# Optimization experiments

Measured on AMD Instinct MI355X. Metric: run time of the kernel, lower is better.

## Reference

```python
import jax, jax.numpy as jnp
import numpy as np

N, F_IN, HID, PERIODS, E = 50000, 8, 64, 12, 1200000


def _lin_init(k, fi, fo):
    # torch.nn.Linear default init: U(-1/sqrt(fi), 1/sqrt(fi))
    s = 1.0 / np.sqrt(fi)
    k1, k2 = jax.random.split(k)
    W = jax.random.uniform(k1, (fi, fo), minval=-s, maxval=s, dtype=jnp.float32)
    b = jax.random.uniform(k2, (fo,), minval=-s, maxval=s, dtype=jnp.float32)
    return W, b


def setup_inputs() -> dict:
    key = jax.random.key(0)
    ks = jax.random.split(key, 12)
    x = jax.random.normal(ks[0], (N, F_IN, PERIODS), dtype=jnp.float32)
    edge_index = jax.random.randint(ks[1], (2, E), 0, N, dtype=jnp.int64)
    edge_attr = jax.random.uniform(ks[2], (E,), dtype=jnp.float32)
    # GCNConv weights (glorot) + zero bias
    def gcn_init(k):
        s = np.sqrt(6.0 / (F_IN + HID))
        W = jax.random.uniform(k, (F_IN, HID), minval=-s, maxval=s, dtype=jnp.float32)
        return W, jnp.zeros((HID,), jnp.float32)
    Wcz, bcz = gcn_init(ks[3])
    Wcr, bcr = gcn_init(ks[4])
    Wch, bch = gcn_init(ks[5])
    # gate linears act on cat([conv_out, H]) -> 2*HID inputs
    Wlz, blz = _lin_init(ks[6], 2 * HID, HID)
    Wlr, blr = _lin_init(ks[7], 2 * HID, HID)
    Wlh, blh = _lin_init(ks[8], 2 * HID, HID)
    # temporal attention logits (uniform init as in A3TGCN)
    attention = jax.random.uniform(ks[9], (PERIODS,), dtype=jnp.float32)
    # outer readout Linear(HID, PERIODS)
    Wout, bout = _lin_init(ks[10], HID, PERIODS)
    return {"x": x, "edge_index": edge_index, "edge_attr": edge_attr,
            "attention": attention,
            "Wcz": Wcz, "bcz": bcz, "Wcr": Wcr, "bcr": bcr, "Wch": Wch, "bch": bch,
            "Wlz": Wlz, "blz": blz, "Wlr": Wlr, "blr": blr, "Wlh": Wlh, "blh": blh,
            "Wout": Wout, "bout": bout}


def reference(x, edge_index, edge_attr, attention,
              Wcz, bcz, Wcr, bcr, Wch, bch,
              Wlz, blz, Wlr, blr, Wlh, blh,
              Wout, bout):
    n = x.shape[0]
    src, dst = edge_index[0], edge_index[1]
    # GCN symmetric normalization with self-loops (self-loop weight = 1)
    deg = jax.ops.segment_sum(edge_attr, dst, num_segments=n) + 1.0
    dinv = jax.lax.rsqrt(deg)                      # [N]
    norm = dinv[src] * edge_attr * dinv[dst]       # [E]
    self_norm = (dinv * dinv)[:, None]             # [N,1]

    def gcn(xt, W, b):
        xw = xt @ W                                # [N,HID]
        agg = jax.ops.segment_sum(xw[src] * norm[:, None], dst, num_segments=n)
        return agg + xw * self_norm + b

    H0 = jnp.zeros((n, Wcz.shape[1]), x.dtype)     # A3TGCN passes H=None each period
    probs = jax.nn.softmax(attention)

    def period_step(acc, inp):
        xt, p = inp                                # xt: [N,F_IN]
        Z = jax.nn.sigmoid(jnp.concatenate([gcn(xt, Wcz, bcz), H0], axis=1) @ Wlz + blz)
        R = jax.nn.sigmoid(jnp.concatenate([gcn(xt, Wcr, bcr), H0], axis=1) @ Wlr + blr)
        Ht = jnp.tanh(jnp.concatenate([gcn(xt, Wch, bch), H0 * R], axis=1) @ Wlh + blh)
        H = Z * H0 + (1.0 - Z) * Ht
        return acc + p * H, None

    xs = jnp.moveaxis(x, 2, 0)                     # [PERIODS, N, F_IN]
    H_accum, _ = jax.lax.scan(period_step, jnp.zeros_like(H0), (xs, probs))
    h = jax.nn.relu(H_accum)
    return h @ Wout + bout                         # [N, PERIODS]
```

## Files before the change

### kernel.cpp

```cpp
#include <hip/hip_runtime.h>
#include <hip/hip_fp16.h>
#include <cmath>

#define F_IN 8
#define PER 12
#define FEAT 96
#define HID 64
#define CAP 64
#define NB 8
#define BINBITS 8
#define NPB 256
#define BINCAP 7168
#define EPB 2048

static inline size_t al256(size_t x) { return (x + 255) & ~(size_t)255; }

__device__ __forceinline__ float frcp(float x) { return __builtin_amdgcn_rcpf(x); }

#define MIX_LO(acc, w, bits) \
    asm("v_fma_mix_f32 %0, %1, %2, %0 op_sel_hi:[0,1,0]" : "+v"(acc) : "v"(w), "v"(bits))
#define MIX_HI(acc, w, bits) \
    asm("v_fma_mix_f32 %0, %1, %2, %0 op_sel:[0,1,0] op_sel_hi:[0,1,0]" : "+v"(acc) : "v"(w), "v"(bits))


__global__ void k_weights(const float* __restrict__ Wcz, const float* __restrict__ bcz,
                          const float* __restrict__ Wch, const float* __restrict__ bch,
                          const float* __restrict__ Wlz, const float* __restrict__ blz,
                          const float* __restrict__ Wlh, const float* __restrict__ blh,
                          const float* __restrict__ att, float* __restrict__ M,
                          int* __restrict__ cursor) {
    int t = threadIdx.x;
    int j = t & 63;
    int w = t >> 6;
    cursor[t] = 0;
#pragma unroll
    for (int q = 0; q < 2; ++q) {
        int f = 2 * w + q;
        float az = 0.f, ah = 0.f;
        for (int k = 0; k < HID; ++k) {
            az = fmaf(Wcz[f * HID + k], Wlz[k * HID + j], az);
            ah = fmaf(Wch[f * HID + k], Wlh[k * HID + j], ah);
        }
        M[f * HID + j] = az;
        M[512 + f * HID + j] = ah;
    }
    if (w == 0) {
        float cz = blz[j], ch = blh[j];
        for (int k = 0; k < HID; ++k) {
            cz = fmaf(bcz[k], Wlz[k * HID + j], cz);
            ch = fmaf(bch[k], Wlh[k * HID + j], ch);
        }
        M[1024 + j] = cz;
        M[1088 + j] = ch;
        if (j < PER) {
            float s = 0.f;
            for (int tt = 0; tt < PER; ++tt) s += expf(att[tt]);
            M[1152 + j] = expf(att[j]) / s;
        }
    }
}


__global__ __launch_bounds__(256) void k_pass1(const int* __restrict__ src, const int* __restrict__ dst,
                                               const float* __restrict__ attr,
                                               int* __restrict__ cursor, int2* __restrict__ binned, int e) {
    __shared__ int hist[256];
    __shared__ int base[256];
    int t = threadIdx.x;
    int blockstart = blockIdx.x * EPB;
    hist[t] = 0;
    __syncthreads();
    int2 ent[8];
    int  br[8];
#pragma unroll
    for (int r = 0; r < 8; ++r) {
        int i = blockstart + r * 256 + t;
        if (i < e) {
            int d = dst[i];
            int b = d >> BINBITS;
            int rank = atomicAdd(&hist[b], 1);
            ent[r].x = src[i] | ((d & 255) << 20);
            ent[r].y = __float_as_int(attr[i]);
            br[r] = (b << 13) | rank;
        } else br[r] = -1;
    }
    __syncthreads();
    int h = hist[t];
    if (h > 0) base[t] = atomicAdd(&cursor[t], h);
    __syncthreads();
#pragma unroll
    for (int r = 0; r < 8; ++r) {
        if (br[r] >= 0) {
            int b = br[r] >> 13, rank = br[r] & 8191;
            int pos = base[b] + rank;
            if (pos < BINCAP)
                binned[(size_t)b * BINCAP + pos] = ent[r];
        }
    }
}


__global__ __launch_bounds__(256) void k_pass2x(const int* __restrict__ cursor, const int2* __restrict__ binned,
                                                const float4* __restrict__ X4,
                                                int2* __restrict__ bucket, int* __restrict__ cnt,
                                                float* __restrict__ dinv_g, uint2* __restrict__ Xh2, int n) {
    __shared__ int   hist[NPB];
    __shared__ float wsum[NPB];
    __shared__ float sdv[NPB];
    int b = blockIdx.x;
    int t = threadIdx.x;
    hist[t] = 0;
    wsum[t] = 0.f;
    __syncthreads();
    int m = min(cursor[b], BINCAP);
    const int2* bin = binned + (size_t)b * BINCAP;
    for (int i = t; i < m; i += 256) {
        int2 p = bin[i];
        int dl = (p.x >> 20) & 255;
        atomicAdd(&wsum[dl], __int_as_float(p.y));
        int rank = atomicAdd(&hist[dl], 1);
        if (rank < CAP) {
            int d = (b << BINBITS) | dl;
            bucket[(size_t)d * CAP + rank] = make_int2(p.x & 0xFFFFF, p.y);
        }
    }
    __syncthreads();
    int node0 = b << BINBITS;
    {
        int node = node0 + t;
        float dv = 0.f;
        if (node < n) {
            cnt[node] = hist[t];
            dv = rsqrtf(1.0f + wsum[t]);
            dinv_g[node] = dv;
        }
        sdv[t] = dv;
    }
    __syncthreads();
    int nn = n - node0; if (nn > NPB) nn = NPB; if (nn < 0) nn = 0;
    int lim = nn * 24;
    size_t base4 = (size_t)node0 * 24;
    for (int i = t; i < lim; i += 256) {
        int nl = i / 24;
        float s = sdv[nl];
        float4 v = X4[base4 + i];
        __half2 a = __floats2half2_rn(s * v.x, s * v.y);
        __half2 c = __floats2half2_rn(s * v.z, s * v.w);
        uint2 o;
        o.x = __builtin_bit_cast(unsigned int, a);
        o.y = __builtin_bit_cast(unsigned int, c);
        Xh2[base4 + i] = o;
    }
}


__global__ void k_zero(int* __restrict__ cnt, int n) {
    int i = blockIdx.x * 256 + threadIdx.x;
    if (i < n) cnt[i] = 0;
}

__global__ void k_bucket(const int* __restrict__ src, const int* __restrict__ dst,
                         const float* __restrict__ attr,
                         int* __restrict__ cnt, int2* __restrict__ bucket, int e) {
    int i = blockIdx.x * 256 + threadIdx.x;
    if (i >= e) return;
    int d = dst[i];
    int pos = atomicAdd(&cnt[d], 1);
    if (pos < CAP) {
        int2 p;
        p.x = src[i];
        p.y = __float_as_int(attr[i]);
        bucket[(size_t)d * CAP + pos] = p;
    }
}

__global__ void k_dinv(const int* __restrict__ cnt, const int2* __restrict__ bucket,
                       float* __restrict__ dinv, int n) {
    int gid = blockIdx.x * 256 + threadIdx.x;
    int node = gid >> 6;
    int lane = gid & 63;
    if (node >= n) return;
    int c = min(cnt[node], CAP);
    float s = (lane < c) ? __int_as_float(bucket[(size_t)node * CAP + lane].y) : 0.f;
#pragma unroll
    for (int d = 32; d; d >>= 1) s += __shfl_xor(s, d);
    if (lane == 0) dinv[node] = rsqrtf(1.0f + s);
}

__global__ void k_xhalf(const float4* __restrict__ X4, const float* __restrict__ dinv,
                        uint2* __restrict__ Xh2, int total4) {
    int i = blockIdx.x * 256 + threadIdx.x;
    if (i >= total4) return;
    int node = i / 24;
    float s = dinv[node];
    float4 v = X4[i];
    __half2 a = __floats2half2_rn(s * v.x, s * v.y);
    __half2 b = __floats2half2_rn(s * v.z, s * v.w);
    uint2 o;
    o.x = __builtin_bit_cast(unsigned int, a);
    o.y = __builtin_bit_cast(unsigned int, b);
    Xh2[i] = o;
}


#define EDGEA(ew, rr)                                  \
    {                                                  \
        float w_ = __int_as_float((ew).y);             \
        MIX_LO(accA0, w_, (rr).x);                     \
        MIX_HI(accA1, w_, (rr).x);                     \
        MIX_LO(accA2, w_, (rr).y);                     \
        MIX_HI(accA3, w_, (rr).y);                     \
    }
#define EDGEB(ew, rr)                                  \
    {                                                  \
        float w_ = __int_as_float((ew).y);             \
        MIX_LO(accB0, w_, (rr).x);                     \
        MIX_HI(accB1, w_, (rr).x);                     \
        MIX_LO(accB2, w_, (rr).y);                     \
        MIX_HI(accB3, w_, (rr).y);                     \
    }

__global__ __launch_bounds__(256) void k_fused(const int* __restrict__ cnt,
                                               const int2* __restrict__ bucket,
                                               const float* __restrict__ dinv,
                                               const uint2* __restrict__ Xh2,
                                               const float* __restrict__ M,
                                               const float* __restrict__ Wout,
                                               const float* __restrict__ bout,
                                               float* __restrict__ out, int n) {
    __shared__ int2  s_ew[NB][CAP];
    __shared__ int   s_cnt[NB];
    __shared__ float s_dv[NB];
    __shared__ float s_xp[NB][104];
    __shared__ float s_acc[NB][HID + 1];
    int t = threadIdx.x;
    int node0 = blockIdx.x * NB;

    if (t < NB) {
        int node = node0 + t;
        s_cnt[t] = (node < n) ? min(cnt[node], CAP) : 0;
        s_dv[t]  = (node < n) ? dinv[node] : 0.f;
    }
    __syncthreads();

#pragma unroll
    for (int idx = t; idx < NB * CAP; idx += 256) {
        int ln = idx >> 6;
        int e  = idx & (CAP - 1);
        if (e < s_cnt[ln]) {
            int2 p = bucket[(size_t)(node0 + ln) * CAP + e];
            s_ew[ln][e] = make_int2(p.x * 24, p.y);
        }
    }
    __syncthreads();

    {
        int g32 = t >> 5;
        int l = t & 31;
        int node = node0 + g32;
        if (node < n && l < 24) {
            float dv = s_dv[g32];
            int c = s_cnt[g32];
            uint2 sh = Xh2[(size_t)node * 24 + l];
            float accA0 = 0.f, accA1 = 0.f, accA2 = 0.f, accA3 = 0.f;
            float accB0 = 0.f, accB1 = 0.f, accB2 = 0.f, accB3 = 0.f;
            int e = 0;
            if (c >= 4) {
                int2  ce0 = s_ew[g32][0], ce1 = s_ew[g32][1], ce2 = s_ew[g32][2], ce3 = s_ew[g32][3];
                uint2 cr0 = Xh2[(size_t)ce0.x + l];
                uint2 cr1 = Xh2[(size_t)ce1.x + l];
                uint2 cr2 = Xh2[(size_t)ce2.x + l];
                uint2 cr3 = Xh2[(size_t)ce3.x + l];
                for (; e + 8 <= c; e += 4) {
                    int2  ne0 = s_ew[g32][e + 4], ne1 = s_ew[g32][e + 5];
                    int2  ne2 = s_ew[g32][e + 6], ne3 = s_ew[g32][e + 7];
                    uint2 nr0 = Xh2[(size_t)ne0.x + l];
                    uint2 nr1 = Xh2[(size_t)ne1.x + l];
                    uint2 nr2 = Xh2[(size_t)ne2.x + l];
                    uint2 nr3 = Xh2[(size_t)ne3.x + l];
                    EDGEA(ce0, cr0); EDGEB(ce1, cr1);
                    EDGEA(ce2, cr2); EDGEB(ce3, cr3);
                    ce0 = ne0; ce1 = ne1; ce2 = ne2; ce3 = ne3;
                    cr0 = nr0; cr1 = nr1; cr2 = nr2; cr3 = nr3;
                }
                EDGEA(ce0, cr0); EDGEB(ce1, cr1);
                EDGEA(ce2, cr2); EDGEB(ce3, cr3);
                e += 4;
            }
            for (; e < c; ++e) {
                int2 e0 = s_ew[g32][e];
                uint2 r0 = Xh2[(size_t)e0.x + l];
                EDGEA(e0, r0);
            }
            float2 sa = __half22float2(__builtin_bit_cast(__half2, sh.x));
            float2 sb = __half22float2(__builtin_bit_cast(__half2, sh.y));
            float4 r;
            r.x = dv * (sa.x + accA0 + accB0);
            r.y = dv * (sa.y + accA1 + accB1);
            r.z = dv * (sb.x + accA2 + accB2);
            r.w = dv * (sb.y + accA3 + accB3);
            *(float4*)&s_xp[g32][l * 4] = r;
        }
    }
    __syncthreads();

    {
        int lane = t & 63;
        int wv = t >> 6;
        float mz[F_IN], mh[F_IN];
#pragma unroll
        for (int f = 0; f < F_IN; ++f) {
            mz[f] = M[f * HID + lane];
            mh[f] = M[512 + f * HID + lane];
        }
        float cz = M[1024 + lane], ch = M[1088 + lane];
        float pr[PER];
#pragma unroll
        for (int tt = 0; tt < PER; ++tt) pr[tt] = M[1152 + tt];

#pragma unroll
        for (int q = 0; q < 2; ++q) {
            int ln = wv * 2 + q;
            if (node0 + ln < n) {
                float acc = 0.f;
#pragma unroll
                for (int tt = 0; tt < PER; ++tt) {
                    float xz = cz, xh = ch;
#pragma unroll
                    for (int f = 0; f < F_IN; ++f) {
                        float xv = s_xp[ln][f * PER + tt];
                        xz = fmaf(xv, mz[f], xz);
                        xh = fmaf(xv, mh[f], xh);
                    }
                    float zb = frcp(1.f + __expf(xz));
                    float th = fmaf(-2.f, frcp(__expf(2.f * xh) + 1.f), 1.f);
                    acc = fmaf(pr[tt], zb * th, acc);
                }
                s_acc[ln][lane] = fmaxf(acc, 0.f);
            }
        }
    }
    __syncthreads();

    if (t < NB * PER) {
        int ln = t / PER;
        int pp = t - ln * PER;
        int node = node0 + ln;
        if (node < n) {
            float o = bout[pp];
#pragma unroll
            for (int j = 0; j < HID; ++j) o = fmaf(s_acc[ln][j], Wout[j * PER + pp], o);
            out[(size_t)node * PER + pp] = o;
        }
    }
}


extern "C" void kernel_launch(void* const* d_in, const int* in_sizes, int n_in,
                              void* d_out, int out_size, void* d_ws, size_t ws_size,
                              hipStream_t stream) {
    const float* X     = (const float*)d_in[0];
    const int*   ei    = (const int*)d_in[1];
    const float* attr  = (const float*)d_in[2];
    const float* att   = (const float*)d_in[3];
    const float* Wcz   = (const float*)d_in[4];
    const float* bcz   = (const float*)d_in[5];
    const float* Wch   = (const float*)d_in[8];
    const float* bch   = (const float*)d_in[9];
    const float* Wlz   = (const float*)d_in[10];
    const float* blz   = (const float*)d_in[11];
    const float* Wlh   = (const float*)d_in[14];
    const float* blh   = (const float*)d_in[15];
    const float* Wout  = (const float*)d_in[16];
    const float* bout  = (const float*)d_in[17];
    float* out = (float*)d_out;

    const int N = in_sizes[0] / FEAT;
    const int E = in_sizes[2];
    const int* src = ei;
    const int* dst = ei + E;

    const int NBINS  = (N + NPB - 1) >> BINBITS;
    const int total4 = N * (FEAT / 4);

    char* base = (char*)d_ws;
    size_t o = 0;
    int*   cnt    = (int*)  (base + o); o += al256((size_t)N * 4);
    float* dinv   = (float*)(base + o); o += al256((size_t)N * 4);
    float* M      = (float*)(base + o); o += al256(1280 * 4);
    int2*  bucket = (int2*) (base + o); o += al256((size_t)N * CAP * 8);
    uint2* Xh2    = (uint2*)(base + o); o += al256((size_t)N * FEAT * 2);
    int*   cursor = (int*)  (base + o); o += al256(256 * 4);
    int2*  binned = (int2*) (base + o);
    size_t need_sorted = o + al256((size_t)NBINS * BINCAP * 8);

    if (ws_size >= need_sorted && NBINS <= 256 && N < (1 << 20)) {
        k_weights<<<1, 256, 0, stream>>>(Wcz, bcz, Wch, bch, Wlz, blz, Wlh, blh, att, M, cursor);
        k_pass1<<<(E + EPB - 1) / EPB, 256, 0, stream>>>(src, dst, attr, cursor, binned, E);
        k_pass2x<<<NBINS, 256, 0, stream>>>(cursor, binned, (const float4*)X, bucket, cnt, dinv, Xh2, N);
    } else {
        k_weights<<<1, 256, 0, stream>>>(Wcz, bcz, Wch, bch, Wlz, blz, Wlh, blh, att, M, cursor);
        k_zero<<<(N + 255) / 256, 256, 0, stream>>>(cnt, N);
        k_bucket<<<(E + 255) / 256, 256, 0, stream>>>(src, dst, attr, cnt, bucket, E);
        k_dinv<<<((N * 64) + 255) / 256, 256, 0, stream>>>(cnt, bucket, dinv, N);
        k_xhalf<<<(total4 + 255) / 256, 256, 0, stream>>>((const float4*)X, dinv, Xh2, total4);
    }

    int blocks = (N + NB - 1) / NB;
    k_fused<<<blocks, 256, 0, stream>>>(cnt, bucket, dinv, Xh2, M, Wout, bout, out, N);
}
```

Measured before the change: 113.7 us.

## Fold log2e into gate weights, merge sigmoid-tanh reciprocals, halve pass1 edges per block

The z and h gate weights and biases are prescaled by log2(e) and 2*log2(e), so the hot loop can call the hardware exp2 directly. It then computes (1-z)*tanh as (B-1)/((1+A)(1+B)), which needs one reciprocal per period instead of two. The self term is folded into the accumulators with fma_mix, dropping the half-to-float conversions. Separately, the binning pass handles 1024 edges per block instead of 2048, launching more blocks with fewer registers each, at the cost of more global cursor atomics. The product (1+A)(1+B) can overflow to inf for large logits, which changes numerical edge behaviour.

After: 120.3 us. 5.8% more time.

```diff
diff --git a/kernel.cpp b/kernel.cpp
--- a/kernel.cpp
+++ b/kernel.cpp
@@ -11,11 +11,13 @@
 #define BINBITS 8
 #define NPB 256
 #define BINCAP 7168
-#define EPB 2048
+#define EPB 1024
+#define LOG2E 1.44269504088896340736f
 
 static inline size_t al256(size_t x) { return (x + 255) & ~(size_t)255; }
 
 __device__ __forceinline__ float frcp(float x) { return __builtin_amdgcn_rcpf(x); }
+__device__ __forceinline__ float fexp2(float x) { return __builtin_amdgcn_exp2f(x); }
 
 #define MIX_LO(acc, w, bits) \
     asm("v_fma_mix_f32 %0, %1, %2, %0 op_sel_hi:[0,1,0]" : "+v"(acc) : "v"(w), "v"(bits))
@@ -41,8 +43,8 @@
             az = fmaf(Wcz[f * HID + k], Wlz[k * HID + j], az);
             ah = fmaf(Wch[f * HID + k], Wlh[k * HID + j], ah);
         }
-        M[f * HID + j] = az;
-        M[512 + f * HID + j] = ah;
+        M[f * HID + j] = az * LOG2E;
+        M[512 + f * HID + j] = ah * (2.0f * LOG2E);
     }
     if (w == 0) {
         float cz = blz[j], ch = blh[j];
@@ -50,8 +52,8 @@
             cz = fmaf(bcz[k], Wlz[k * HID + j], cz);
             ch = fmaf(bch[k], Wlh[k * HID + j], ch);
         }
-        M[1024 + j] = cz;
-        M[1088 + j] = ch;
+        M[1024 + j] = cz * LOG2E;
+        M[1088 + j] = ch * (2.0f * LOG2E);
         if (j < PER) {
             float s = 0.f;
             for (int tt = 0; tt < PER; ++tt) s += expf(att[tt]);
@@ -70,10 +72,10 @@
     int blockstart = blockIdx.x * EPB;
     hist[t] = 0;
     __syncthreads();
-    int2 ent[8];
-    int  br[8];
-#pragma unroll
-    for (int r = 0; r < 8; ++r) {
+    int2 ent[4];
+    int  br[4];
+#pragma unroll
+    for (int r = 0; r < 4; ++r) {
         int i = blockstart + r * 256 + t;
         if (i < e) {
             int d = dst[i];
@@ -89,7 +91,7 @@
     if (h > 0) base[t] = atomicAdd(&cursor[t], h);
     __syncthreads();
 #pragma unroll
-    for (int r = 0; r < 8; ++r) {
+    for (int r = 0; r < 4; ++r) {
         if (br[r] >= 0) {
             int b = br[r] >> 13, rank = br[r] & 8191;
             int pos = base[b] + rank;
@@ -264,6 +266,13 @@
             uint2 sh = Xh2[(size_t)node * 24 + l];
             float accA0 = 0.f, accA1 = 0.f, accA2 = 0.f, accA3 = 0.f;
             float accB0 = 0.f, accB1 = 0.f, accB2 = 0.f, accB3 = 0.f;
+            {
+                float one = 1.0f;
+                MIX_LO(accA0, one, sh.x);
+                MIX_HI(accA1, one, sh.x);
+                MIX_LO(accA2, one, sh.y);
+                MIX_HI(accA3, one, sh.y);
+            }
             int e = 0;
             if (c >= 4) {
                 int2  ce0 = s_ew[g32][0], ce1 = s_ew[g32][1], ce2 = s_ew[g32][2], ce3 = s_ew[g32][3];
@@ -292,13 +301,11 @@
                 uint2 r0 = Xh2[(size_t)e0.x + l];
                 EDGEA(e0, r0);
             }
-            float2 sa = __half22float2(__builtin_bit_cast(__half2, sh.x));
-            float2 sb = __half22float2(__builtin_bit_cast(__half2, sh.y));
             float4 r;
-            r.x = dv * (sa.x + accA0 + accB0);
-            r.y = dv * (sa.y + accA1 + accB1);
-            r.z = dv * (sb.x + accA2 + accB2);
-            r.w = dv * (sb.y + accA3 + accB3);
+            r.x = dv * (accA0 + accB0);
+            r.y = dv * (accA1 + accB1);
+            r.z = dv * (accA2 + accB2);
+            r.w = dv * (accA3 + accB3);
             *(float4*)&s_xp[g32][l * 4] = r;
         }
     }
@@ -332,9 +339,10 @@
                         xz = fmaf(xv, mz[f], xz);
                         xh = fmaf(xv, mh[f], xh);
                     }
-                    float zb = frcp(1.f + __expf(xz));
-                    float th = fmaf(-2.f, frcp(__expf(2.f * xh) + 1.f), 1.f);
-                    acc = fmaf(pr[tt], zb * th, acc);
+                    float A = fexp2(xz);
+                    float B = fexp2(xh);
+                    float r = frcp((1.f + A) * (1.f + B));
+                    acc = fmaf(pr[tt] * (B - 1.f), r, acc);
                 }
                 s_acc[ln][lane] = fmaxf(acc, 0.f);
             }
```
